# Performance work log

Measured on AMD Instinct MI355X. Metric: run time of the kernel, lower is better.

## Reference

```python
import jax, jax.numpy as jnp
import numpy as np

VOXEL_SIZE = np.array([0.32, 0.32, 6.0], dtype=np.float32)
SPATIAL_SIZE = np.array([-74.88, 74.88, -74.88, 74.88, -3.0, 3.0], dtype=np.float32)
# voxel_spatial_size = ceil((max-min)/voxel_size) per dim -> [468, 468, 1]
GRID = np.array([int(np.ceil((SPATIAL_SIZE[2*i+1]-SPATIAL_SIZE[2*i])/VOXEL_SIZE[i])) for i in range(3)], dtype=np.int32)
# voxel origin = floor(min / voxel_size) -> [-234, -234, -1]
ORIGIN = np.floor(SPATIAL_SIZE[0::2] / VOXEL_SIZE).astype(np.int32)
VOL = int(np.prod(GRID))  # 468*468*1
# row-major id multipliers: prods[1:]+[1] -> [468, 1, 1]
SHIFT = np.array([int(np.prod(GRID[1:])), int(np.prod(GRID[2:])), 1], dtype=np.int32)
VOXEL_FEATURE_MIN = -1000.0

B, N, D_IN, MLP = 4, 100000, 16, 128


def setup_inputs() -> dict:
    key = jax.random.key(0)
    k1, k2, k3, k4, k5 = jax.random.split(key, 5)
    xy = jax.random.uniform(k1, (B, N, 2), minval=-80.0, maxval=80.0)
    z = jax.random.uniform(k2, (B, N, 1), minval=-4.0, maxval=4.0)
    point_xyz = jnp.concatenate([xy, z], axis=-1)
    point_feature = jax.random.normal(k3, (B, N, D_IN), dtype=jnp.float32)
    point_mask = jax.random.uniform(k4, (B, N)) < 0.95
    W = jax.random.normal(k5, (D_IN + 3, MLP), dtype=jnp.float32) * 0.1
    b = jnp.zeros((MLP,), dtype=jnp.float32)
    return {"point_xyz": point_xyz, "point_feature": point_feature,
            "point_mask": point_mask, "W": W, "b": b}


def reference(point_xyz, point_feature, point_mask, W, b):
    vs = jnp.asarray(VOXEL_SIZE, dtype=point_xyz.dtype)
    # PointToVoxel
    pvx_f = jnp.floor(point_xyz / vs)                      # [B,N,3] float voxel coords
    point_voxel_feature = point_xyz - pvx_f * vs           # delta within voxel
    pvx = pvx_f.astype(jnp.int32) - jnp.asarray(ORIGIN)    # shifted int voxel coords
    grid = jnp.asarray(GRID)
    in_bounds = jnp.all((pvx >= 0) & (pvx < grid), axis=-1)
    voxel_mask = in_bounds & point_mask                    # [B,N]
    vid = jnp.sum(pvx * jnp.asarray(SHIFT), axis=-1)       # [B,N]
    vid = vid + jnp.arange(B, dtype=jnp.int32)[:, None] * VOL
    vid = vid * voxel_mask.astype(jnp.int32)               # invalid -> 0
    # point net (Dense + ReLU) on [point_feature, voxel delta]
    feat = jnp.concatenate([point_feature, point_voxel_feature], axis=-1)
    mf = voxel_mask.astype(feat.dtype)[..., None]
    feat = feat * mf
    feat = jax.nn.relu(jnp.einsum('bnd,dk->bnk', feat, W) + b)
    feat = feat * mf
    # scatter-max into dense voxel grid
    seg = jax.ops.segment_max(feat.reshape(-1, MLP), vid.reshape(-1),
                              num_segments=B * VOL)
    seg = jnp.where(seg > VOXEL_FEATURE_MIN, seg, 0.0)
    # z dim is 1 -> squeezed: [B, 468, 468, MLP]
    return seg.reshape(B, int(GRID[0]), int(GRID[1]), MLP)
```

## Files before the change

### kernel.cpp

```cpp
#include <hip/hip_runtime.h>
#include <stdint.h>

#define BB   4
#define NN   100000
#define TOTAL (BB * NN)
#define DIN  16
#define DF   19
#define KO   128
#define GX   468
#define GY   468
#define VOL  (GX * GY)
#define NV   (BB * VOL)
#define CAP  12
#define SLOT_F 20
#define NWAVES (NV / 64)
#define OUT_F4 ((size_t)NV * KO / 4)

typedef float vfloat2 __attribute__((ext_vector_type(2)));

#define WS_COUNTS   0
#define WS_FLAG     (NV)
#define WS_PACKED   (NV + 16)

__global__ __launch_bounds__(256) void fill_prep(
    float4* __restrict__ out4,
    int4* __restrict__ counts4,
    const uint4* __restrict__ mask_words,
    int* __restrict__ flag)
{
    if (blockIdx.x == 0) {
        __shared__ int sA, sB;
        if (threadIdx.x == 0) { sA = 0; sB = 0; }
        __syncthreads();
        int a = 0, b = 0;
        #pragma unroll
        for (int it = 0; it < 4; ++it) {
            uint4 w = mask_words[it * 256 + threadIdx.x];
            unsigned lo = (w.x & 0xFFu) | (w.y & 0xFFu) | (w.z & 0xFFu) | (w.w & 0xFFu);
            unsigned hi = (w.x & 0xFFFFFF00u) | (w.y & 0xFFFFFF00u) |
                          (w.z & 0xFFFFFF00u) | (w.w & 0xFFFFFF00u);
            if (hi) a = 1;
            if (lo) b = 1;
        }
        if (a) atomicOr(&sA, 1);
        if (b) atomicOr(&sB, 1);
        __syncthreads();
        if (threadIdx.x == 0) flag[0] = (sA && sB) ? 1 : 4;
    }
    const unsigned t0 = blockIdx.x * 256 + threadIdx.x;
    const unsigned stride = gridDim.x * 256;
    const int4 zi = make_int4(0, 0, 0, 0);
    for (unsigned i = t0; i < NV / 4; i += stride) counts4[i] = zi;
    const float4 zf = make_float4(0.f, 0.f, 0.f, 0.f);
    for (size_t i = t0; i < OUT_F4; i += stride) out4[i] = zf;
}

__global__ __launch_bounds__(256) void pass1_bin(
    const float* __restrict__ xyz,
    const float* __restrict__ pfeat,
    const unsigned char* __restrict__ mask_raw,
    const int* __restrict__ flag,
    int* __restrict__ counts,
    float* __restrict__ packed)
{
    const int p = blockIdx.x * 256 + threadIdx.x;
    if (p >= TOTAL) return;
    const float x = xyz[p * 3 + 0];
    const float y = xyz[p * 3 + 1];
    const float z = xyz[p * 3 + 2];
    bool m;
    if (flag[0] == 4) m = (((const int*)mask_raw)[p] != 0);
    else              m = (mask_raw[p] != 0);
    const float fx = floorf(x / 0.32f);
    const float fy = floorf(y / 0.32f);
    const float fz = floorf(z / 6.0f);
    const int ix = (int)fx + 234;
    const int iy = (int)fy + 234;
    const int iz = (int)fz + 1;
    const bool inb = ((unsigned)ix < (unsigned)GX) &
                     ((unsigned)iy < (unsigned)GY) &
                     (iz == 0) & m;
    if (!inb) return;
    const int vid = (p / NN) * VOL + ix * GY + iy;
    const int rank = atomicAdd(&counts[vid], 1);
    if (rank >= CAP) return;

    float4* slot = (float4*)(packed + (size_t)(vid * CAP + rank) * SLOT_F);
    const float4* pf4 = (const float4*)(pfeat + (size_t)p * DIN);
    slot[0] = pf4[0];
    slot[1] = pf4[1];
    slot[2] = pf4[2];
    slot[3] = pf4[3];
    slot[4] = make_float4(x - fx * 0.32f, y - fy * 0.32f, z - fz * 6.0f, 0.f);
}

__global__ __launch_bounds__(256) void write_occ(
    const float* __restrict__ W,
    const float* __restrict__ bias,
    const int* __restrict__ counts,
    const float* __restrict__ packed,
    float* __restrict__ out)
{
    const int lane = threadIdx.x & 63;
    const int wid  = (blockIdx.x * 256 + threadIdx.x) >> 6;
    if (wid >= NWAVES) return;
    const int v0 = wid * 64;

    const int c_mine = counts[v0 + lane];
    const unsigned long long occ = __ballot(c_mine > 0);
    if (!occ) return;

    const float2* W2 = (const float2*)W;
    float2 w[DF];
    #pragma unroll
    for (int d = 0; d < DF; ++d) w[d] = W2[d * 64 + lane];
    const float2 bb = ((const float2*)bias)[lane];

    vfloat2* dst0 = (vfloat2*)(out + (size_t)v0 * KO) + lane;

    unsigned long long rem = occ;
    int j_cur = __builtin_ctzll(rem);
    rem &= rem - 1;
    float4 q0, q1, q2, q3, q4;
    {
        const float4* base = (const float4*)(packed +
                             (size_t)(v0 + j_cur) * CAP * SLOT_F);
        q0 = base[0]; q1 = base[1]; q2 = base[2]; q3 = base[3]; q4 = base[4];
    }
    while (j_cur >= 0) {
        int j_nxt = -1;
        float4 n0, n1, n2, n3, n4;
        if (rem) {
            j_nxt = __builtin_ctzll(rem);
            rem &= rem - 1;
            const float4* nb = (const float4*)(packed +
                               (size_t)(v0 + j_nxt) * CAP * SLOT_F);
            n0 = nb[0]; n1 = nb[1]; n2 = nb[2]; n3 = nb[3]; n4 = nb[4];
        }

        const int c = min(__shfl(c_mine, j_cur), CAP);
        const float4* base = (const float4*)(packed +
                             (size_t)(v0 + j_cur) * CAP * SLOT_F);
        float m0 = -3.0e38f, m1 = -3.0e38f;
        for (int t = 0; t < c; ++t) {
            float4 p0, p1, p2, p3, p4;
            if (t == 0) { p0 = q0; p1 = q1; p2 = q2; p3 = q3; p4 = q4; }
            else {
                p0 = base[t * 5 + 0]; p1 = base[t * 5 + 1];
                p2 = base[t * 5 + 2]; p3 = base[t * 5 + 3];
                p4 = base[t * 5 + 4];
            }
            float a0 = bb.x, a1 = bb.y;
            a0 = fmaf(p0.x, w[0].x, a0);  a1 = fmaf(p0.x, w[0].y, a1);
            a0 = fmaf(p0.y, w[1].x, a0);  a1 = fmaf(p0.y, w[1].y, a1);
            a0 = fmaf(p0.z, w[2].x, a0);  a1 = fmaf(p0.z, w[2].y, a1);
            a0 = fmaf(p0.w, w[3].x, a0);  a1 = fmaf(p0.w, w[3].y, a1);
            a0 = fmaf(p1.x, w[4].x, a0);  a1 = fmaf(p1.x, w[4].y, a1);
            a0 = fmaf(p1.y, w[5].x, a0);  a1 = fmaf(p1.y, w[5].y, a1);
            a0 = fmaf(p1.z, w[6].x, a0);  a1 = fmaf(p1.z, w[6].y, a1);
            a0 = fmaf(p1.w, w[7].x, a0);  a1 = fmaf(p1.w, w[7].y, a1);
            a0 = fmaf(p2.x, w[8].x, a0);  a1 = fmaf(p2.x, w[8].y, a1);
            a0 = fmaf(p2.y, w[9].x, a0);  a1 = fmaf(p2.y, w[9].y, a1);
            a0 = fmaf(p2.z, w[10].x, a0); a1 = fmaf(p2.z, w[10].y, a1);
            a0 = fmaf(p2.w, w[11].x, a0); a1 = fmaf(p2.w, w[11].y, a1);
            a0 = fmaf(p3.x, w[12].x, a0); a1 = fmaf(p3.x, w[12].y, a1);
            a0 = fmaf(p3.y, w[13].x, a0); a1 = fmaf(p3.y, w[13].y, a1);
            a0 = fmaf(p3.z, w[14].x, a0); a1 = fmaf(p3.z, w[14].y, a1);
            a0 = fmaf(p3.w, w[15].x, a0); a1 = fmaf(p3.w, w[15].y, a1);
            a0 = fmaf(p4.x, w[16].x, a0); a1 = fmaf(p4.x, w[16].y, a1);
            a0 = fmaf(p4.y, w[17].x, a0); a1 = fmaf(p4.y, w[17].y, a1);
            a0 = fmaf(p4.z, w[18].x, a0); a1 = fmaf(p4.z, w[18].y, a1);
            m0 = fmaxf(m0, a0);
            m1 = fmaxf(m1, a1);
        }
        vfloat2 rv = {fmaxf(m0, 0.f), fmaxf(m1, 0.f)};
        __builtin_nontemporal_store(rv, dst0 + (size_t)j_cur * 64);

        j_cur = j_nxt;
        q0 = n0; q1 = n1; q2 = n2; q3 = n3; q4 = n4;
    }
}

extern "C" void kernel_launch(void* const* d_in, const int* in_sizes, int n_in,
                              void* d_out, int out_size, void* d_ws, size_t ws_size,
                              hipStream_t stream) {
    const float* xyz   = (const float*)d_in[0];
    const float* pfeat = (const float*)d_in[1];
    const unsigned char* mask = (const unsigned char*)d_in[2];
    const float* W     = (const float*)d_in[3];
    const float* bias  = (const float*)d_in[4];
    float* out = (float*)d_out;
    int* ws = (int*)d_ws;

    int*   counts = ws + WS_COUNTS;
    int*   flag   = ws + WS_FLAG;
    float* packed = (float*)(ws + WS_PACKED);

    fill_prep<<<2048, 256, 0, stream>>>((float4*)out, (int4*)counts,
                                        (const uint4*)mask, flag);
    pass1_bin<<<(TOTAL + 255) / 256, 256, 0, stream>>>(xyz, pfeat, mask, flag,
                                                       counts, packed);
    write_occ<<<(NWAVES + 3) / 4, 256, 0, stream>>>(W, bias, counts,
                                                    packed, out);
}
```

Before: 554.5 us.

## Overlap output zero-fill with point binning in one combined kernel

The large zero-fill of the output grid moves out of the prep kernel and into the binning kernel as extra blocks, so the memory-bound fill runs alongside the atomic binning of points. The prep kernel now only clears the counts and sets the mask flag, using one thread per int4 instead of a grid-stride loop. The fill blocks write four float4 each and are launched after the binning blocks. This adds a large block count to the middle kernel and relies on the hardware interleaving the two kinds of block.

```diff
diff --git a/kernel.cpp b/kernel.cpp
--- a/kernel.cpp
+++ b/kernel.cpp
@@ -14,7 +14,10 @@
 #define CAP  12
 #define SLOT_F 20
 #define NWAVES (NV / 64)
-#define OUT_F4 ((size_t)NV * KO / 4)
+#define OUT_F4 (NV * (KO / 4))
+#define FPT   4
+#define FILLB (OUT_F4 / (256 * FPT))
+#define BINB  ((TOTAL + 255) / 256)
 
 typedef float vfloat2 __attribute__((ext_vector_type(2)));
 
@@ -22,8 +25,7 @@
 #define WS_FLAG     (NV)
 #define WS_PACKED   (NV + 16)
 
-__global__ __launch_bounds__(256) void fill_prep(
-    float4* __restrict__ out4,
+__global__ __launch_bounds__(256) void vx_prep(
     int4* __restrict__ counts4,
     const uint4* __restrict__ mask_words,
     int* __restrict__ flag)
@@ -47,15 +49,12 @@
         __syncthreads();
         if (threadIdx.x == 0) flag[0] = (sA && sB) ? 1 : 4;
     }
-    const unsigned t0 = blockIdx.x * 256 + threadIdx.x;
-    const unsigned stride = gridDim.x * 256;
-    const int4 zi = make_int4(0, 0, 0, 0);
-    for (unsigned i = t0; i < NV / 4; i += stride) counts4[i] = zi;
-    const float4 zf = make_float4(0.f, 0.f, 0.f, 0.f);
-    for (size_t i = t0; i < OUT_F4; i += stride) out4[i] = zf;
-}
-
-__global__ __launch_bounds__(256) void pass1_bin(
+    const unsigned i = blockIdx.x * 256 + threadIdx.x;
+    if (i < NV / 4) counts4[i] = make_int4(0, 0, 0, 0);
+}
+
+__global__ __launch_bounds__(256) void vx_stage(
+    float4* __restrict__ out4,
     const float* __restrict__ xyz,
     const float* __restrict__ pfeat,
     const unsigned char* __restrict__ mask_raw,
@@ -63,7 +62,18 @@
     int* __restrict__ counts,
     float* __restrict__ packed)
 {
-    const int p = blockIdx.x * 256 + threadIdx.x;
+    const unsigned b = blockIdx.x;
+    if (b >= (unsigned)BINB) {
+        const unsigned base = ((b - BINB) * 256 + threadIdx.x) * FPT;
+        const float4 zf = make_float4(0.f, 0.f, 0.f, 0.f);
+        #pragma unroll
+        for (int k = 0; k < FPT; ++k) {
+            const unsigned idx = base + k;
+            if (idx < (unsigned)OUT_F4) out4[idx] = zf;
+        }
+        return;
+    }
+    const int p = (int)(b * 256 + threadIdx.x);
     if (p >= TOTAL) return;
     const float x = xyz[p * 3 + 0];
     const float y = xyz[p * 3 + 1];
@@ -94,7 +104,7 @@
     slot[4] = make_float4(x - fx * 0.32f, y - fy * 0.32f, z - fz * 6.0f, 0.f);
 }
 
-__global__ __launch_bounds__(256) void write_occ(
+__global__ __launch_bounds__(256) void vx_write(
     const float* __restrict__ W,
     const float* __restrict__ bias,
     const int* __restrict__ counts,
@@ -196,10 +206,10 @@
     int*   flag   = ws + WS_FLAG;
     float* packed = (float*)(ws + WS_PACKED);
 
-    fill_prep<<<2048, 256, 0, stream>>>((float4*)out, (int4*)counts,
-                                        (const uint4*)mask, flag);
-    pass1_bin<<<(TOTAL + 255) / 256, 256, 0, stream>>>(xyz, pfeat, mask, flag,
-                                                       counts, packed);
-    write_occ<<<(NWAVES + 3) / 4, 256, 0, stream>>>(W, bias, counts,
-                                                    packed, out);
-}
+    vx_prep<<<(NV / 4 + 255) / 256, 256, 0, stream>>>((int4*)counts,
+                                                      (const uint4*)mask, flag);
+    vx_stage<<<BINB + FILLB, 256, 0, stream>>>((float4*)out, xyz, pfeat,
+                                               mask, flag, counts, packed);
+    vx_write<<<(NWAVES + 3) / 4, 256, 0, stream>>>(W, bias, counts,
+                                                   packed, out);
+}
```

Measured after the change: 593.2 us. 7.0% more time.
